# Kernel tuning notes

Measured on AMD Instinct MI355X. Metric: run time of the kernel, lower is better.

The kernel has to match this reference:

```python
import jax, jax.numpy as jnp
import numpy as np

B, C, NA = 32, 9, 65440
GAMMA = 3.0
SCALE_XY = 1.0 / 0.1
SCALE_WH = 1.0 / 0.2


def setup_inputs() -> dict:
    key = jax.random.key(0)
    k1, k2, k3, k4, k5 = jax.random.split(key, 5)
    bbox_delta = jax.random.normal(k1, (B, 4, NA), dtype=jnp.float32)
    confs = jax.random.normal(k2, (B, C, NA), dtype=jnp.float32)
    # gt boxes in xywh, keep w/h strictly positive for the log() in _loc_vec
    gt_bbox = jax.random.uniform(k3, (B, NA, 4), dtype=jnp.float32, minval=0.05, maxval=1.0)
    gt_labels = jax.random.randint(k4, (B, NA), 0, C, dtype=jnp.int32)
    anchors = jax.random.uniform(k5, (1, 4, NA), dtype=jnp.float32, minval=0.1, maxval=1.0)
    return {"bbox_delta": bbox_delta, "confs": confs, "gt_bbox": gt_bbox,
            "gt_labels": gt_labels, "anchors": anchors}


def reference(bbox_delta, confs, gt_bbox, gt_labels, anchors):
    n_classes = confs.shape[1]
    # ---- focal classification loss (fused: no one-hot materialized) ----
    # alpha = [10, 1000, ..., 1000]; einsum 'a,bcd->bad' followed by sum(dim=1)
    # collapses to multiplying by sum(alpha) since y is one-hot over c.
    alpha = jnp.full((n_classes,), 1000.0, dtype=jnp.float32).at[0].set(10.0)
    logp = jax.nn.log_softmax(confs, axis=1)              # [B,C,N]
    t = gt_labels.astype(jnp.int32)[:, None, :]           # [B,1,N]
    logp_t = jnp.take_along_axis(logp, t, axis=1)[:, 0, :]  # [B,N]
    p_t = jnp.exp(logp_t)
    focal = (1.0 - p_t) ** GAMMA * logp_t                 # [B,N]
    classification_loss = jnp.mean(-jnp.sum(alpha) * focal)

    # ---- localization loss (masked smooth-L1, no boolean compaction) ----
    gt_t = jnp.transpose(gt_bbox, (0, 2, 1))               # [B,4,N]
    gxy = SCALE_XY * (gt_t[:, :2, :] - anchors[:, :2, :]) / anchors[:, 2:, :]
    gwh = SCALE_WH * jnp.log(gt_t[:, 2:, :] / anchors[:, 2:, :])
    gt_loc = jnp.concatenate([gxy, gwh], axis=1)           # [B,4,N]

    pos = gt_labels > 0                                    # [B,N]
    mask = pos[:, None, :]                                 # broadcast over 4 coords
    diff = jnp.where(mask, bbox_delta - gt_loc, 0.0)
    ad = jnp.abs(diff)
    sl1 = jnp.where(ad < 1.0, 0.5 * diff * diff, ad - 0.5)
    regression_loss = jnp.sum(jnp.where(mask, sl1, 0.0))
    num_pos = jnp.sum(pos).astype(jnp.float32)

    total_loss = regression_loss / num_pos + classification_loss
    return total_loss
```

## Files before the change

kernel.cpp:

```cpp
#include <hip/hip_runtime.h>
#include <math.h>

constexpr int B  = 32;
constexpr int C  = 9;
constexpr int NA = 65440;
constexpr int PER_B    = NA / 4;
constexpr int NTHREADS = B * PER_B;
constexpr int BLOCK    = 256;
constexpr int GRID     = NTHREADS / BLOCK;

constexpr int WS_REG = 2048;
constexpr int WS_POS = 4096;

__device__ __forceinline__ float4 ld4(const float* p) {
    return *reinterpret_cast<const float4*>(p);
}

__device__ __forceinline__ float smooth_l1(float d) {
    float ad = fabsf(d);
    return ad < 1.0f ? 0.5f * d * d : ad - 0.5f;
}

__global__ __launch_bounds__(BLOCK, 4) void ssd_main(
    const float* __restrict__ bbox_delta,
    const float* __restrict__ confs,
    const float* __restrict__ gt_bbox,
    const int*   __restrict__ gt_labels,
    const float* __restrict__ anchors,
    float* __restrict__ ws)
{
    const int tid = blockIdx.x * BLOCK + threadIdx.x;
    const int b   = tid / PER_B;
    const int a   = (tid - b * PER_B) * 4;

    const float* cbase = confs + (size_t)b * C * NA + a;
    float4 cf0 = ld4(cbase);
    float4 cf1 = ld4(cbase + 1 * NA);
    float4 cf2 = ld4(cbase + 2 * NA);
    float4 cf3 = ld4(cbase + 3 * NA);
    float4 cf4 = ld4(cbase + 4 * NA);
    float4 cf5 = ld4(cbase + 5 * NA);
    float4 cf6 = ld4(cbase + 6 * NA);
    float4 cf7 = ld4(cbase + 7 * NA);
    float4 cf8 = ld4(cbase + 8 * NA);

    const int4 lab = *reinterpret_cast<const int4*>(gt_labels + (size_t)b * NA + a);

    const float* abase = anchors + a;
    float4 ax = ld4(abase);
    float4 ay = ld4(abase + NA);
    float4 aw = ld4(abase + 2 * NA);
    float4 ah = ld4(abase + 3 * NA);

    const float* dbase = bbox_delta + (size_t)b * 4 * NA + a;
    float4 d0 = ld4(dbase);
    float4 d1 = ld4(dbase + NA);
    float4 d2 = ld4(dbase + 2 * NA);
    float4 d3 = ld4(dbase + 3 * NA);

    const float* gbase = gt_bbox + ((size_t)b * NA + a) * 4;
    float4 g0 = ld4(gbase);
    float4 g1 = ld4(gbase + 4);
    float4 g2 = ld4(gbase + 8);
    float4 g3 = ld4(gbase + 12);

    __builtin_amdgcn_sched_barrier(0);

    float4 cf[C] = {cf0, cf1, cf2, cf3, cf4, cf5, cf6, cf7, cf8};
    float sex = 0.f, sey = 0.f, sez = 0.f, sew = 0.f;
    float ctx = cf0.x, cty = cf0.y, ctz = cf0.z, ctw = cf0.w;
#pragma unroll
    for (int c = 0; c < C; ++c) {
        sex += __expf(cf[c].x);
        sey += __expf(cf[c].y);
        sez += __expf(cf[c].z);
        sew += __expf(cf[c].w);
        ctx = (lab.x == c) ? cf[c].x : ctx;
        cty = (lab.y == c) ? cf[c].y : cty;
        ctz = (lab.z == c) ? cf[c].z : ctz;
        ctw = (lab.w == c) ? cf[c].w : ctw;
    }
    float lpx = ctx - __logf(sex);
    float lpy = cty - __logf(sey);
    float lpz = ctz - __logf(sez);
    float lpw = ctw - __logf(sew);

    float focal;
    {
        float px = __expf(lpx), py = __expf(lpy), pz = __expf(lpz), pw = __expf(lpw);
        float ox = 1.f - px, oy = 1.f - py, oz = 1.f - pz, ow = 1.f - pw;
        focal = ox*ox*ox*lpx + oy*oy*oy*lpy + oz*oz*oz*lpz + ow*ow*ow*lpw;
    }

    float reg = 0.f, pcnt = 0.f;
#define DO_ANCHOR(GT, AXC, AYC, AWC, AHC, D0C, D1C, D2C, D3C, LABC)               \
    {                                                                             \
        float gx = 10.0f * __fdividef(GT.x - AXC, AWC);                           \
        float gy = 10.0f * __fdividef(GT.y - AYC, AHC);                           \
        float gw = 5.0f * __logf(__fdividef(GT.z, AWC));                          \
        float gh = 5.0f * __logf(__fdividef(GT.w, AHC));                          \
        float s  = smooth_l1(D0C - gx) + smooth_l1(D1C - gy) +                    \
                   smooth_l1(D2C - gw) + smooth_l1(D3C - gh);                     \
        if (LABC > 0) { reg += s; pcnt += 1.0f; }                                 \
    }
    DO_ANCHOR(g0, ax.x, ay.x, aw.x, ah.x, d0.x, d1.x, d2.x, d3.x, lab.x)
    DO_ANCHOR(g1, ax.y, ay.y, aw.y, ah.y, d0.y, d1.y, d2.y, d3.y, lab.y)
    DO_ANCHOR(g2, ax.z, ay.z, aw.z, ah.z, d0.z, d1.z, d2.z, d3.z, lab.z)
    DO_ANCHOR(g3, ax.w, ay.w, aw.w, ah.w, d0.w, d1.w, d2.w, d3.w, lab.w)
#undef DO_ANCHOR

#pragma unroll
    for (int off = 32; off > 0; off >>= 1) {
        focal += __shfl_down(focal, off, 64);
        reg   += __shfl_down(reg,   off, 64);
        pcnt  += __shfl_down(pcnt,  off, 64);
    }
    __shared__ float sf[4], sr[4], sp[4];
    const int wid  = threadIdx.x >> 6;
    const int lane = threadIdx.x & 63;
    if (lane == 0) { sf[wid] = focal; sr[wid] = reg; sp[wid] = pcnt; }
    __syncthreads();
    if (threadIdx.x == 0) {
        ws[blockIdx.x]          = sf[0] + sf[1] + sf[2] + sf[3];
        ws[WS_REG + blockIdx.x] = sr[0] + sr[1] + sr[2] + sr[3];
        ws[WS_POS + blockIdx.x] = sp[0] + sp[1] + sp[2] + sp[3];
    }
}

__global__ __launch_bounds__(256) void finalize_k(const float* __restrict__ ws,
                                                  float* __restrict__ out) {
    float F = 0.f, R = 0.f, P = 0.f;
    for (int i = threadIdx.x; i < GRID; i += 256) {
        F += ws[i];
        R += ws[WS_REG + i];
        P += ws[WS_POS + i];
    }
#pragma unroll
    for (int off = 32; off > 0; off >>= 1) {
        F += __shfl_down(F, off, 64);
        R += __shfl_down(R, off, 64);
        P += __shfl_down(P, off, 64);
    }
    __shared__ float sf[4], sr[4], sp[4];
    const int wid  = threadIdx.x >> 6;
    const int lane = threadIdx.x & 63;
    if (lane == 0) { sf[wid] = F; sr[wid] = R; sp[wid] = P; }
    __syncthreads();
    if (threadIdx.x == 0) {
        float Ft = sf[0] + sf[1] + sf[2] + sf[3];
        float Rt = sr[0] + sr[1] + sr[2] + sr[3];
        float Pt = sp[0] + sp[1] + sp[2] + sp[3];
        const float inv_n = 1.0f / (float)((size_t)B * NA);
        out[0] = Rt / Pt - 8010.0f * Ft * inv_n;
    }
}

extern "C" void kernel_launch(void* const* d_in, const int* in_sizes, int n_in,
                              void* d_out, int out_size, void* d_ws, size_t ws_size,
                              hipStream_t stream) {
    const float* bbox_delta = (const float*)d_in[0];
    const float* confs      = (const float*)d_in[1];
    const float* gt_bbox    = (const float*)d_in[2];
    const int*   gt_labels  = (const int*)d_in[3];
    const float* anchors    = (const float*)d_in[4];
    float* ws  = (float*)d_ws;
    float* out = (float*)d_out;

    ssd_main<<<GRID, BLOCK, 0, stream>>>(bbox_delta, confs, gt_bbox, gt_labels, anchors, ws);
    finalize_k<<<1, 256, 0, stream>>>(ws, out);
}
```

Before: 174.3 us.

## Stream class logits into LDS via async global_load_lds, overlap with regression math

Class-logit loads now use asynchronous global-to-LDS loads (16 bytes per lane) instead of being loaded straight into registers. They are issued after the other loads, and the smooth-L1 localization math runs while they are in flight. After an explicit vmcnt wait, each thread reads its logits back from LDS for the softmax/focal part. This is meant to cut vector register pressure and overlap memory latency with compute. In exchange it uses 36KB of LDS per block, which may limit occupancy, and adds a round trip through LDS.

```diff
diff --git a/kernel.cpp b/kernel.cpp
--- a/kernel.cpp
+++ b/kernel.cpp
@@ -21,6 +21,9 @@
     return ad < 1.0f ? 0.5f * d * d : ad - 0.5f;
 }
 
+typedef __attribute__((address_space(3))) void       lds_void_t;
+typedef const __attribute__((address_space(1))) void gbl_void_t;
+
 __global__ __launch_bounds__(BLOCK, 4) void ssd_main(
     const float* __restrict__ bbox_delta,
     const float* __restrict__ confs,
@@ -29,20 +32,12 @@
     const float* __restrict__ anchors,
     float* __restrict__ ws)
 {
+    __shared__ float conf_lds[C][BLOCK * 4];
+
     const int tid = blockIdx.x * BLOCK + threadIdx.x;
     const int b   = tid / PER_B;
     const int a   = (tid - b * PER_B) * 4;
-
-    const float* cbase = confs + (size_t)b * C * NA + a;
-    float4 cf0 = ld4(cbase);
-    float4 cf1 = ld4(cbase + 1 * NA);
-    float4 cf2 = ld4(cbase + 2 * NA);
-    float4 cf3 = ld4(cbase + 3 * NA);
-    float4 cf4 = ld4(cbase + 4 * NA);
-    float4 cf5 = ld4(cbase + 5 * NA);
-    float4 cf6 = ld4(cbase + 6 * NA);
-    float4 cf7 = ld4(cbase + 7 * NA);
-    float4 cf8 = ld4(cbase + 8 * NA);
+    const int wid = threadIdx.x >> 6;
 
     const int4 lab = *reinterpret_cast<const int4*>(gt_labels + (size_t)b * NA + a);
 
@@ -66,9 +61,43 @@
 
     __builtin_amdgcn_sched_barrier(0);
 
-    float4 cf[C] = {cf0, cf1, cf2, cf3, cf4, cf5, cf6, cf7, cf8};
+    const float* cg = confs + (size_t)b * C * NA + a;
+#pragma unroll
+    for (int c = 0; c < C; ++c) {
+        __builtin_amdgcn_global_load_lds(
+            (gbl_void_t*)(cg + (size_t)c * NA),
+            (lds_void_t*)(&conf_lds[c][wid * 256]),
+            16, 0, 0);
+    }
+    __builtin_amdgcn_sched_barrier(0);
+
+    float reg = 0.f, pcnt = 0.f;
+#define DO_ANCHOR(GT, AXC, AYC, AWC, AHC, D0C, D1C, D2C, D3C, LABC)               \
+    {                                                                             \
+        float gx = 10.0f * __fdividef(GT.x - AXC, AWC);                           \
+        float gy = 10.0f * __fdividef(GT.y - AYC, AHC);                           \
+        float gw = 5.0f * __logf(__fdividef(GT.z, AWC));                          \
+        float gh = 5.0f * __logf(__fdividef(GT.w, AHC));                          \
+        float s  = smooth_l1(D0C - gx) + smooth_l1(D1C - gy) +                    \
+                   smooth_l1(D2C - gw) + smooth_l1(D3C - gh);                     \
+        if (LABC > 0) { reg += s; pcnt += 1.0f; }                                 \
+    }
+    DO_ANCHOR(g0, ax.x, ay.x, aw.x, ah.x, d0.x, d1.x, d2.x, d3.x, lab.x)
+    DO_ANCHOR(g1, ax.y, ay.y, aw.y, ah.y, d0.y, d1.y, d2.y, d3.y, lab.y)
+    DO_ANCHOR(g2, ax.z, ay.z, aw.z, ah.z, d0.z, d1.z, d2.z, d3.z, lab.z)
+    DO_ANCHOR(g3, ax.w, ay.w, aw.w, ah.w, d0.w, d1.w, d2.w, d3.w, lab.w)
+#undef DO_ANCHOR
+
+    asm volatile("s_waitcnt vmcnt(0)" ::: "memory");
+    __builtin_amdgcn_sched_barrier(0);
+
+    float4 cf[C];
+#pragma unroll
+    for (int c = 0; c < C; ++c)
+        cf[c] = *reinterpret_cast<const float4*>(&conf_lds[c][threadIdx.x * 4]);
+
     float sex = 0.f, sey = 0.f, sez = 0.f, sew = 0.f;
-    float ctx = cf0.x, cty = cf0.y, ctz = cf0.z, ctw = cf0.w;
+    float ctx = cf[0].x, cty = cf[0].y, ctz = cf[0].z, ctw = cf[0].w;
 #pragma unroll
     for (int c = 0; c < C; ++c) {
         sex += __expf(cf[c].x);
@@ -92,23 +121,6 @@
         focal = ox*ox*ox*lpx + oy*oy*oy*lpy + oz*oz*oz*lpz + ow*ow*ow*lpw;
     }
 
-    float reg = 0.f, pcnt = 0.f;
-#define DO_ANCHOR(GT, AXC, AYC, AWC, AHC, D0C, D1C, D2C, D3C, LABC)               \
-    {                                                                             \
-        float gx = 10.0f * __fdividef(GT.x - AXC, AWC);                           \
-        float gy = 10.0f * __fdividef(GT.y - AYC, AHC);                           \
-        float gw = 5.0f * __logf(__fdividef(GT.z, AWC));                          \
-        float gh = 5.0f * __logf(__fdividef(GT.w, AHC));                          \
-        float s  = smooth_l1(D0C - gx) + smooth_l1(D1C - gy) +                    \
-                   smooth_l1(D2C - gw) + smooth_l1(D3C - gh);                     \
-        if (LABC > 0) { reg += s; pcnt += 1.0f; }                                 \
-    }
-    DO_ANCHOR(g0, ax.x, ay.x, aw.x, ah.x, d0.x, d1.x, d2.x, d3.x, lab.x)
-    DO_ANCHOR(g1, ax.y, ay.y, aw.y, ah.y, d0.y, d1.y, d2.y, d3.y, lab.y)
-    DO_ANCHOR(g2, ax.z, ay.z, aw.z, ah.z, d0.z, d1.z, d2.z, d3.z, lab.z)
-    DO_ANCHOR(g3, ax.w, ay.w, aw.w, ah.w, d0.w, d1.w, d2.w, d3.w, lab.w)
-#undef DO_ANCHOR
-
 #pragma unroll
     for (int off = 32; off > 0; off >>= 1) {
         focal += __shfl_down(focal, off, 64);
@@ -116,7 +128,6 @@
         pcnt  += __shfl_down(pcnt,  off, 64);
     }
     __shared__ float sf[4], sr[4], sp[4];
-    const int wid  = threadIdx.x >> 6;
     const int lane = threadIdx.x & 63;
     if (lane == 0) { sf[wid] = focal; sr[wid] = reg; sp[wid] = pcnt; }
     __syncthreads();
```

New measurement: 172.6 us. About the same (-1.0%).
